# Performance work log

Hardware: AMD Instinct MI355X
Metric: run time of the kernel (lower is better)

Reference implementation:

```python
import jax, jax.numpy as jnp
import numpy as np

N = 100000
E = 3200000
D_IN = 512
D_HID = 128
D_OUT = 4


def setup_inputs() -> dict:
    key = jax.random.key(0)
    k1, k2, k3, k4, k5, k6 = jax.random.split(key, 6)
    x = jax.random.normal(k1, (N, D_IN), dtype=jnp.float32)
    edge_index = jax.random.randint(k2, (2, E), 0, N, dtype=jnp.int64)
    # GCNConv params (Glorot-ish scale)
    W1 = jax.random.normal(k3, (D_IN, D_HID), dtype=jnp.float32) / np.sqrt(D_IN)
    b1 = jax.random.normal(k4, (D_HID,), dtype=jnp.float32) * 0.01
    W2 = jax.random.normal(k5, (D_HID, D_OUT), dtype=jnp.float32) / np.sqrt(D_HID)
    b2 = jax.random.normal(k6, (D_OUT,), dtype=jnp.float32) * 0.01
    return {"x": x, "edge_index": edge_index, "W1": W1, "b1": b1, "W2": W2, "b2": b2}


def _gcn_conv(x, W, b, src, dst, deg_inv_sqrt):
    # h = X W, then symmetric-normalized aggregation with self-loops (PyG GCNConv default)
    h = x @ W                                   # [N, F_out]
    norm = deg_inv_sqrt[src] * deg_inv_sqrt[dst]  # [E]
    agg = jax.ops.segment_sum(h[src] * norm[:, None], dst, num_segments=x.shape[0])
    # self-loop contribution: norm_ii = deg_inv_sqrt[i]^2
    agg = agg + h * (deg_inv_sqrt ** 2)[:, None]
    return agg + b


def reference(x, edge_index, W1, b1, W2, b2):
    src, dst = edge_index[0], edge_index[1]
    # degree with added self-loops (edge weights = 1)
    deg = jax.ops.segment_sum(jnp.ones((E,), dtype=x.dtype), dst, num_segments=N) + 1.0
    deg_inv_sqrt = jax.lax.rsqrt(deg)
    h = jax.nn.relu(_gcn_conv(x, W1, b1, src, dst, deg_inv_sqrt))
    out = _gcn_conv(h, W2, b2, src, dst, deg_inv_sqrt)
    return out
```

## Files before the change

kernel.cpp:

```cpp
#include <hip/hip_runtime.h>
#include <hip/hip_fp16.h>

#define DIN 512
#define DHID 128
#define DOUT 4
#define BSH 8
#define PA_CHUNK 8192
#define AST 72

typedef _Float16 f16x8 __attribute__((ext_vector_type(8)));
typedef _Float16 f16x4 __attribute__((ext_vector_type(4)));
typedef float    f32x4 __attribute__((ext_vector_type(4)));

__global__ void detect_i64_k(const int* __restrict__ raw, int* __restrict__ flag) {
  if (blockIdx.x == 0 && threadIdx.x == 0) {
    int z = 1;
    for (int k = 0; k < 8; ++k)
      if (raw[2 * k + 1] != 0) z = 0;
    flag[0] = z;
  }
}

__global__ __launch_bounds__(256) void bcount_k(const int* __restrict__ raw,
                                                const int* __restrict__ flag,
                                                int* __restrict__ gbcnt, int E) {
  __shared__ int h[512];
  const int tid = threadIdx.x;
  const int f = flag[0];
  for (int i = tid; i < 512; i += 256) h[i] = 0;
  __syncthreads();
  const size_t e0 = (size_t)blockIdx.x * PA_CHUNK;
  #pragma unroll
  for (int k = 0; k < 32; ++k) {
    size_t e = e0 + (size_t)k * 256 + tid;
    if (e < (size_t)E) {
      int d = f ? raw[2 * ((size_t)E + e)] : raw[(size_t)E + e];
      atomicAdd(&h[d >> BSH], 1);
    }
  }
  __syncthreads();
  for (int i = tid; i < 512; i += 256)
    if (h[i]) atomicAdd(&gbcnt[i], h[i]);
}

__global__ __launch_bounds__(512) void bscan_k(const int* __restrict__ gbcnt,
                                               int* __restrict__ boffs,
                                               int* __restrict__ bcur,
                                               int* __restrict__ offs,
                                               int nbkt, int N, int E) {
  __shared__ int sm[512];
  int t = threadIdx.x;
  int v = (t < nbkt) ? gbcnt[t] : 0;
  int x = v;
  sm[t] = x;
  __syncthreads();
  #pragma unroll
  for (int o = 1; o < 512; o <<= 1) {
    int y = (t >= o) ? sm[t - o] : 0;
    __syncthreads();
    x += y;
    sm[t] = x;
    __syncthreads();
  }
  if (t < nbkt) {
    boffs[t] = x - v;
    bcur[t] = x - v;
  }
  if (t == 0) {
    boffs[nbkt] = E;
    offs[N] = E;
  }
}

__global__ __launch_bounds__(256) void binA_k(const int* __restrict__ raw,
                                              const int* __restrict__ flag,
                                              int* __restrict__ bcur,
                                              unsigned* __restrict__ pairs, int E) {
  __shared__ int hist[512];
  __shared__ int base[512];
  const int tid = threadIdx.x;
  const int f = flag[0];
  const size_t e0 = (size_t)blockIdx.x * PA_CHUNK;
  for (int i = tid; i < 512; i += 256) hist[i] = 0;
  __syncthreads();
  int es[32], ed[32];
  #pragma unroll
  for (int k = 0; k < 32; ++k) {
    size_t e = e0 + (size_t)k * 256 + tid;
    if (e < (size_t)E) {
      es[k] = f ? raw[2 * e] : raw[e];
      ed[k] = f ? raw[2 * ((size_t)E + e)] : raw[(size_t)E + e];
      atomicAdd(&hist[ed[k] >> BSH], 1);
    } else {
      ed[k] = -1;
    }
  }
  __syncthreads();
  for (int i = tid; i < 512; i += 256) {
    int c = hist[i];
    base[i] = c ? atomicAdd(&bcur[i], c) : 0;
    hist[i] = 0;
  }
  __syncthreads();
  #pragma unroll
  for (int k = 0; k < 32; ++k) {
    if (ed[k] >= 0) {
      int b = ed[k] >> BSH;
      int pos = base[b] + atomicAdd(&hist[b], 1);
      pairs[pos] = ((unsigned)es[k] << 8) | ((unsigned)ed[k] & 255u);
    }
  }
}

__global__ __launch_bounds__(256) void binB_k(const unsigned* __restrict__ pairs,
                                              const int* __restrict__ boffs,
                                              int* __restrict__ csr,
                                              int* __restrict__ offs,
                                              float* __restrict__ dis, int N) {
  __shared__ int lcnt[256];
  __shared__ int sc[256];
  const int tid = threadIdx.x;
  const int n0 = blockIdx.x << BSH;
  const int lo = boffs[blockIdx.x];
  const int hi = boffs[blockIdx.x + 1];
  lcnt[tid] = 0;
  __syncthreads();
  for (int j = lo + tid; j < hi; j += 256) atomicAdd(&lcnt[(int)(pairs[j] & 255u)], 1);
  __syncthreads();
  int v = lcnt[tid];
  int x = v;
  sc[tid] = x;
  __syncthreads();
  #pragma unroll
  for (int o = 1; o < 256; o <<= 1) {
    int y = (tid >= o) ? sc[tid - o] : 0;
    __syncthreads();
    x += y;
    sc[tid] = x;
    __syncthreads();
  }
  const int base = lo + x - v;
  const int node = n0 + tid;
  if (node < N) {
    offs[node] = base;
    dis[node] = rsqrtf((float)v + 1.0f);
  }
  __syncthreads();
  lcnt[tid] = base;
  __syncthreads();
  for (int j = lo + tid; j < hi; j += 256) {
    unsigned p = pairs[j];
    int dl = (int)(p & 255u);
    int pos = atomicAdd(&lcnt[dl], 1);
    csr[pos] = (int)(p >> 8);
  }
}

__global__ __launch_bounds__(256) void wsplit_k(const float* __restrict__ W1,
                                                __half* __restrict__ Wth,
                                                __half* __restrict__ Wtl) {
  int idx = blockIdx.x * 256 + threadIdx.x;
  if (idx >= DIN * DHID) return;
  int k = idx >> 7;
  int n = idx & 127;
  float w = W1[idx];
  _Float16 hi = (_Float16)w;
  _Float16 lo = (_Float16)(w - (float)hi);
  Wth[(size_t)n * DIN + k] = *(__half*)&hi;
  Wtl[(size_t)n * DIN + k] = *(__half*)&lo;
}

__global__ __launch_bounds__(256, 2) void gemm1_k(const float* __restrict__ A,
                                                  const __half* __restrict__ Bth,
                                                  const __half* __restrict__ Btl,
                                                  const float* __restrict__ dis,
                                                  __half* __restrict__ hs, int N) {
  __shared__ _Float16 smem[4 * 128 * AST];
  __shared__ float sdis[128];
  _Float16* sAh = smem;
  _Float16* sAl = smem + 128 * AST;
  _Float16* sBh = smem + 2 * 128 * AST;
  _Float16* sBl = smem + 3 * 128 * AST;
  const int tid = threadIdx.x;
  const int wave = tid >> 6, lane = tid & 63;
  const int lr = lane & 15, quad = lane >> 4;
  const int m0 = blockIdx.x * 128;
  const int mbase = (wave >> 1) * 64;
  const int nbase = (wave & 1) * 64;
  if (tid < 128) sdis[tid] = (m0 + tid < N) ? dis[m0 + tid] : 0.f;

  f32x4 acc[4][4];
  #pragma unroll
  for (int mt = 0; mt < 4; ++mt)
    #pragma unroll
    for (int nt = 0; nt < 4; ++nt) acc[mt][nt] = (f32x4){0.f, 0.f, 0.f, 0.f};

  for (int k0 = 0; k0 < DIN; k0 += 64) {
    #pragma unroll
    for (int l = 0; l < 8; ++l) {
      int idx = l * 256 + tid;
      int row = idx >> 4;
      int kk = (idx & 15) << 2;
      int gr = m0 + row;
      float4 v = make_float4(0.f, 0.f, 0.f, 0.f);
      if (gr < N) v = *(const float4*)(A + (size_t)gr * DIN + k0 + kk);
      _Float16 h0 = (_Float16)v.x, h1 = (_Float16)v.y,
               h2 = (_Float16)v.z, h3 = (_Float16)v.w;
      f16x4 hi4 = {h0, h1, h2, h3};
      f16x4 lo4 = {(_Float16)(v.x - (float)h0), (_Float16)(v.y - (float)h1),
                   (_Float16)(v.z - (float)h2), (_Float16)(v.w - (float)h3)};
      *(f16x4*)&sAh[row * AST + kk] = hi4;
      *(f16x4*)&sAl[row * AST + kk] = lo4;
    }
    #pragma unroll
    for (int l = 0; l < 4; ++l) {
      int idx = l * 256 + tid;
      int row = idx >> 3;
      int kk = (idx & 7) << 3;
      *(f16x8*)&sBh[row * AST + kk] =
          *(const f16x8*)(Bth + (size_t)row * DIN + k0 + kk);
      *(f16x8*)&sBl[row * AST + kk] =
          *(const f16x8*)(Btl + (size_t)row * DIN + k0 + kk);
    }
    __syncthreads();
    #pragma unroll
    for (int ks = 0; ks < 2; ++ks) {
      const int ko = ks * 32 + quad * 8;
      f16x8 ah[4], al[4];
      #pragma unroll
      for (int mt = 0; mt < 4; ++mt) {
        int r = mbase + mt * 16 + lr;
        ah[mt] = *(const f16x8*)&sAh[r * AST + ko];
        al[mt] = *(const f16x8*)&sAl[r * AST + ko];
      }
      #pragma unroll
      for (int nt = 0; nt < 4; ++nt) {
        int c = nbase + nt * 16 + lr;
        f16x8 bh = *(const f16x8*)&sBh[c * AST + ko];
        f16x8 bl = *(const f16x8*)&sBl[c * AST + ko];
        #pragma unroll
        for (int mt = 0; mt < 4; ++mt) {
          acc[mt][nt] = __builtin_amdgcn_mfma_f32_16x16x32_f16(al[mt], bh, acc[mt][nt], 0, 0, 0);
          acc[mt][nt] = __builtin_amdgcn_mfma_f32_16x16x32_f16(ah[mt], bl, acc[mt][nt], 0, 0, 0);
          acc[mt][nt] = __builtin_amdgcn_mfma_f32_16x16x32_f16(ah[mt], bh, acc[mt][nt], 0, 0, 0);
        }
      }
    }
    __syncthreads();
  }
  #pragma unroll
  for (int mt = 0; mt < 4; ++mt) {
    #pragma unroll
    for (int nt = 0; nt < 4; ++nt) {
      int col = nbase + nt * 16 + lr;
      #pragma unroll
      for (int r = 0; r < 4; ++r) {
        int row = mbase + mt * 16 + quad * 4 + r;
        smem[row * 136 + col] = (_Float16)(acc[mt][nt][r] * sdis[row]);
      }
    }
  }
  __syncthreads();
  #pragma unroll
  for (int l = 0; l < 8; ++l) {
    int idx = l * 256 + tid;
    int row = idx >> 4;
    int c = (idx & 15) << 3;
    int gr = m0 + row;
    if (gr < N)
      *(uint4*)(hs + (size_t)gr * DHID + c) = *(uint4*)&smem[row * 136 + c];
  }
}

__global__ __launch_bounds__(256) void agg1_k(const __half* __restrict__ hs,
                                              const float* __restrict__ dis,
                                              const int* __restrict__ offs,
                                              const int* __restrict__ csr,
                                              const float* __restrict__ W2,
                                              const float* __restrict__ b1,
                                              float* __restrict__ gs, int N) {
  const int wid = threadIdx.x >> 6;
  const int lane = threadIdx.x & 63;
  const int i = blockIdx.x * 4 + wid;
  if (i >= N) return;
  const int f = lane * 2;
  const __half* hp = hs + f;
  float ax = 0.f, ay = 0.f;
  const int beg = offs[i], end = offs[i + 1];
  for (int base = beg; base < end; base += 64) {
    int sj = 0;
    if (base + lane < end) sj = csr[base + lane];
    const int n = min(64, end - base);
    int t = 0;
    for (; t + 8 <= n; t += 8) {
      int s0 = __shfl(sj, t + 0, 64), s1 = __shfl(sj, t + 1, 64);
      int s2 = __shfl(sj, t + 2, 64), s3 = __shfl(sj, t + 3, 64);
      int s4 = __shfl(sj, t + 4, 64), s5 = __shfl(sj, t + 5, 64);
      int s6 = __shfl(sj, t + 6, 64), s7 = __shfl(sj, t + 7, 64);
      __half2 h0 = *(const __half2*)(hp + (size_t)s0 * DHID);
      __half2 h1 = *(const __half2*)(hp + (size_t)s1 * DHID);
      __half2 h2 = *(const __half2*)(hp + (size_t)s2 * DHID);
      __half2 h3 = *(const __half2*)(hp + (size_t)s3 * DHID);
      __half2 h4 = *(const __half2*)(hp + (size_t)s4 * DHID);
      __half2 h5 = *(const __half2*)(hp + (size_t)s5 * DHID);
      __half2 h6 = *(const __half2*)(hp + (size_t)s6 * DHID);
      __half2 h7 = *(const __half2*)(hp + (size_t)s7 * DHID);
      float2 f0 = __half22float2(h0), f1 = __half22float2(h1);
      float2 f2 = __half22float2(h2), f3 = __half22float2(h3);
      float2 f4 = __half22float2(h4), f5 = __half22float2(h5);
      float2 f6 = __half22float2(h6), f7 = __half22float2(h7);
      ax += ((f0.x + f1.x) + (f2.x + f3.x)) + ((f4.x + f5.x) + (f6.x + f7.x));
      ay += ((f0.y + f1.y) + (f2.y + f3.y)) + ((f4.y + f5.y) + (f6.y + f7.y));
    }
    for (; t < n; ++t) {
      int s = __shfl(sj, t, 64);
      float2 hf = __half22float2(*(const __half2*)(hp + (size_t)s * DHID));
      ax += hf.x;
      ay += hf.y;
    }
  }
  {
    float2 hf = __half22float2(*(const __half2*)(hp + (size_t)i * DHID));
    ax += hf.x;
    ay += hf.y;
  }
  const float di = dis[i];
  float v0 = fmaxf(fmaf(ax, di, b1[f]), 0.f);
  float v1 = fmaxf(fmaf(ay, di, b1[f + 1]), 0.f);
  float p0 = fmaf(v0, W2[f * 4 + 0], v1 * W2[f * 4 + 4]);
  float p1 = fmaf(v0, W2[f * 4 + 1], v1 * W2[f * 4 + 5]);
  float p2 = fmaf(v0, W2[f * 4 + 2], v1 * W2[f * 4 + 6]);
  float p3 = fmaf(v0, W2[f * 4 + 3], v1 * W2[f * 4 + 7]);
  #pragma unroll
  for (int o = 32; o > 0; o >>= 1) {
    p0 += __shfl_xor(p0, o, 64);
    p1 += __shfl_xor(p1, o, 64);
    p2 += __shfl_xor(p2, o, 64);
    p3 += __shfl_xor(p3, o, 64);
  }
  if (lane == 0)
    *(float4*)(gs + (size_t)i * DOUT) = make_float4(p0 * di, p1 * di, p2 * di, p3 * di);
}

__global__ __launch_bounds__(256) void agg2_k(const float* __restrict__ gs,
                                              const float* __restrict__ dis,
                                              const int* __restrict__ offs,
                                              const int* __restrict__ csr,
                                              const float* __restrict__ b2,
                                              float* __restrict__ out, int N) {
  int i = blockIdx.x * 256 + threadIdx.x;
  if (i >= N) return;
  float a0 = 0.f, a1 = 0.f, a2 = 0.f, a3 = 0.f;
  const int beg = offs[i], end = offs[i + 1];
  int j = beg;
  for (; j + 4 <= end; j += 4) {
    int s0 = csr[j], s1 = csr[j + 1], s2 = csr[j + 2], s3 = csr[j + 3];
    float4 g0 = *(const float4*)(gs + (size_t)s0 * DOUT);
    float4 g1 = *(const float4*)(gs + (size_t)s1 * DOUT);
    float4 g2 = *(const float4*)(gs + (size_t)s2 * DOUT);
    float4 g3 = *(const float4*)(gs + (size_t)s3 * DOUT);
    a0 += (g0.x + g1.x) + (g2.x + g3.x);
    a1 += (g0.y + g1.y) + (g2.y + g3.y);
    a2 += (g0.z + g1.z) + (g2.z + g3.z);
    a3 += (g0.w + g1.w) + (g2.w + g3.w);
  }
  for (; j < end; ++j) {
    int s = csr[j];
    float4 gv = *(const float4*)(gs + (size_t)s * DOUT);
    a0 += gv.x; a1 += gv.y; a2 += gv.z; a3 += gv.w;
  }
  const float di = dis[i];
  float4 gi = *(const float4*)(gs + (size_t)i * DOUT);
  float4 o4;
  o4.x = fmaf(a0 + gi.x, di, b2[0]);
  o4.y = fmaf(a1 + gi.y, di, b2[1]);
  o4.z = fmaf(a2 + gi.z, di, b2[2]);
  o4.w = fmaf(a3 + gi.w, di, b2[3]);
  *(float4*)(out + (size_t)i * DOUT) = o4;
}

extern "C" void kernel_launch(void* const* d_in, const int* in_sizes, int n_in,
                              void* d_out, int out_size, void* d_ws, size_t ws_size,
                              hipStream_t stream) {
  const float* x  = (const float*)d_in[0];
  const int*   raw = (const int*)d_in[1];
  const float* W1 = (const float*)d_in[2];
  const float* b1 = (const float*)d_in[3];
  const float* W2 = (const float*)d_in[4];
  const float* b2 = (const float*)d_in[5];
  float* out = (float*)d_out;

  const int N = in_sizes[0] / DIN;
  const int E = in_sizes[1] / 2;

  char* ws = (char*)d_ws;
  size_t off = 0;
  auto carve = [&](size_t bytes) -> char* {
    char* p = ws + off;
    off = (off + bytes + 255) & ~(size_t)255;
    return p;
  };
  float*    dis  = (float*)carve((size_t)N * 4);
  int*      offs = (int*)carve((size_t)(N + 1) * 4);
  int*      csr  = (int*)carve((size_t)E * 4);
  unsigned* pairs= (unsigned*)carve((size_t)E * 4);
  int*      boffs= (int*)carve(513 * 4);
  int*      bcur = (int*)carve(512 * 4);
  int*      gbcnt= (int*)carve(512 * 4);
  int*      flag = (int*)carve(256);
  __half*   Wth  = (__half*)carve((size_t)DIN * DHID * 2);
  __half*   Wtl  = (__half*)carve((size_t)DIN * DHID * 2);
  __half*   hs   = (__half*)carve((size_t)N * DHID * 2);
  float*    gs   = (float*)carve((size_t)N * DOUT * 4);
  (void)ws_size; (void)n_in; (void)out_size;

  const int gN = (N + 255) / 256;
  const int nbkt = (N + (1 << BSH) - 1) >> BSH;
  const int gA = (E + PA_CHUNK - 1) / PA_CHUNK;

  detect_i64_k<<<1, 64, 0, stream>>>(raw, flag);
  hipMemsetAsync(gbcnt, 0, 512 * 4, stream);
  bcount_k<<<gA, 256, 0, stream>>>(raw, flag, gbcnt, E);
  bscan_k<<<1, 512, 0, stream>>>(gbcnt, boffs, bcur, offs, nbkt, N, E);
  binA_k<<<gA, 256, 0, stream>>>(raw, flag, bcur, pairs, E);
  binB_k<<<nbkt, 256, 0, stream>>>(pairs, boffs, csr, offs, dis, N);
  wsplit_k<<<(DIN * DHID + 255) / 256, 256, 0, stream>>>(W1, Wth, Wtl);
  gemm1_k<<<(N + 127) / 128, 256, 0, stream>>>(x, Wth, Wtl, dis, hs, N);
  agg1_k<<<(N + 3) / 4, 256, 0, stream>>>(hs, dis, offs, csr, W2, b1, gs, N);
  agg2_k<<<gN, 256, 0, stream>>>(gs, dis, offs, csr, b2, out, N);
}
```

Measured before the change: 571.5 us.

## Register-prefetch next K-slice in gemm1 with smaller tiles for higher occupancy

The GEMM1 K-step drops from 64 to 32, which shrinks the LDS tiles (BST 40) and raises launch bounds to 3 blocks per CU. Global loads for the next K-slice go into registers before the MFMA work on the current slice, so memory latency overlaps compute. The dis shared buffer is removed and dis is read straight from global in the epilogue. In exchange there are twice as many barriers per K loop and more register pressure, which could cause spills under the 3-block bound.

```diff
diff --git a/kernel.cpp b/kernel.cpp
--- a/kernel.cpp
+++ b/kernel.cpp
@@ -6,7 +6,7 @@
 #define DOUT 4
 #define BSH 8
 #define PA_CHUNK 8192
-#define AST 72
+#define BST 40
 
 typedef _Float16 f16x8 __attribute__((ext_vector_type(8)));
 typedef _Float16 f16x4 __attribute__((ext_vector_type(4)));
@@ -170,24 +170,50 @@
   Wtl[(size_t)n * DIN + k] = *(__half*)&lo;
 }
 
-__global__ __launch_bounds__(256, 2) void gemm1_k(const float* __restrict__ A,
+#define STAGE_A(v, l)                                                          \
+  {                                                                            \
+    _Float16 h0 = (_Float16)(v).x, h1 = (_Float16)(v).y,                       \
+             h2 = (_Float16)(v).z, h3 = (_Float16)(v).w;                       \
+    f16x4 hi4 = {h0, h1, h2, h3};                                              \
+    f16x4 lo4 = {(_Float16)((v).x - (float)h0), (_Float16)((v).y - (float)h1), \
+                 (_Float16)((v).z - (float)h2), (_Float16)((v).w - (float)h3)};\
+    *(f16x4*)&sAh[((l) * 32 + ar) * BST + akk] = hi4;                          \
+    *(f16x4*)&sAl[((l) * 32 + ar) * BST + akk] = lo4;                          \
+  }
+
+__global__ __launch_bounds__(256, 3) void gemm1_k(const float* __restrict__ A,
                                                   const __half* __restrict__ Bth,
                                                   const __half* __restrict__ Btl,
                                                   const float* __restrict__ dis,
                                                   __half* __restrict__ hs, int N) {
-  __shared__ _Float16 smem[4 * 128 * AST];
-  __shared__ float sdis[128];
+  __shared__ _Float16 smem[4 * 128 * BST];
   _Float16* sAh = smem;
-  _Float16* sAl = smem + 128 * AST;
-  _Float16* sBh = smem + 2 * 128 * AST;
-  _Float16* sBl = smem + 3 * 128 * AST;
+  _Float16* sAl = smem + 128 * BST;
+  _Float16* sBh = smem + 2 * 128 * BST;
+  _Float16* sBl = smem + 3 * 128 * BST;
   const int tid = threadIdx.x;
   const int wave = tid >> 6, lane = tid & 63;
   const int lr = lane & 15, quad = lane >> 4;
   const int m0 = blockIdx.x * 128;
   const int mbase = (wave >> 1) * 64;
   const int nbase = (wave & 1) * 64;
-  if (tid < 128) sdis[tid] = (m0 + tid < N) ? dis[m0 + tid] : 0.f;
+
+  const int ar  = tid >> 3;
+  const int akk = (tid & 7) << 2;
+  const int br0 = tid >> 2;
+  const int br1 = (256 + tid) >> 2;
+  const int bcc = (tid & 3) << 3;
+
+  const int g0 = m0 + ar,      g1 = m0 + 32 + ar;
+  const int g2 = m0 + 64 + ar, g3 = m0 + 96 + ar;
+  const float* a0p = A + (size_t)g0 * DIN + akk;
+  const float* a1p = A + (size_t)g1 * DIN + akk;
+  const float* a2p = A + (size_t)g2 * DIN + akk;
+  const float* a3p = A + (size_t)g3 * DIN + akk;
+  const __half* bh0p = Bth + (size_t)br0 * DIN + bcc;
+  const __half* bh1p = Bth + (size_t)br1 * DIN + bcc;
+  const __half* bl0p = Btl + (size_t)br0 * DIN + bcc;
+  const __half* bl1p = Btl + (size_t)br1 * DIN + bcc;
 
   f32x4 acc[4][4];
   #pragma unroll
@@ -195,68 +221,73 @@
     #pragma unroll
     for (int nt = 0; nt < 4; ++nt) acc[mt][nt] = (f32x4){0.f, 0.f, 0.f, 0.f};
 
-  for (int k0 = 0; k0 < DIN; k0 += 64) {
+  const float4 z4 = make_float4(0.f, 0.f, 0.f, 0.f);
+  float4 pa0 = (g0 < N) ? *(const float4*)a0p : z4;
+  float4 pa1 = (g1 < N) ? *(const float4*)a1p : z4;
+  float4 pa2 = (g2 < N) ? *(const float4*)a2p : z4;
+  float4 pa3 = (g3 < N) ? *(const float4*)a3p : z4;
+  uint4 pbh0 = *(const uint4*)bh0p;
+  uint4 pbh1 = *(const uint4*)bh1p;
+  uint4 pbl0 = *(const uint4*)bl0p;
+  uint4 pbl1 = *(const uint4*)bl1p;
+
+  for (int k0 = 0; k0 < DIN; k0 += 32) {
+    STAGE_A(pa0, 0);
+    STAGE_A(pa1, 1);
+    STAGE_A(pa2, 2);
+    STAGE_A(pa3, 3);
+    *(uint4*)&sBh[br0 * BST + bcc] = pbh0;
+    *(uint4*)&sBh[br1 * BST + bcc] = pbh1;
+    *(uint4*)&sBl[br0 * BST + bcc] = pbl0;
+    *(uint4*)&sBl[br1 * BST + bcc] = pbl1;
+    __syncthreads();
+    if (k0 + 32 < DIN) {
+      const int k1 = k0 + 32;
+      pa0 = (g0 < N) ? *(const float4*)(a0p + k1) : z4;
+      pa1 = (g1 < N) ? *(const float4*)(a1p + k1) : z4;
+      pa2 = (g2 < N) ? *(const float4*)(a2p + k1) : z4;
+      pa3 = (g3 < N) ? *(const float4*)(a3p + k1) : z4;
+      pbh0 = *(const uint4*)(bh0p + k1);
+      pbh1 = *(const uint4*)(bh1p + k1);
+      pbl0 = *(const uint4*)(bl0p + k1);
+      pbl1 = *(const uint4*)(bl1p + k1);
+    }
+    const int ko = quad * 8;
+    f16x8 ah[4], al[4];
     #pragma unroll
-    for (int l = 0; l < 8; ++l) {
-      int idx = l * 256 + tid;
-      int row = idx >> 4;
-      int kk = (idx & 15) << 2;
+    for (int mt = 0; mt < 4; ++mt) {
+      int r = mbase + mt * 16 + lr;
+      ah[mt] = *(const f16x8*)&sAh[r * BST + ko];
+      al[mt] = *(const f16x8*)&sAl[r * BST + ko];
+    }
+    #pragma unroll
+    for (int nt = 0; nt < 4; ++nt) {
+      int c = nbase + nt * 16 + lr;
+      f16x8 bh = *(const f16x8*)&sBh[c * BST + ko];
+      f16x8 bl = *(const f16x8*)&sBl[c * BST + ko];
+      #pragma unroll
+      for (int mt = 0; mt < 4; ++mt)
+        acc[mt][nt] = __builtin_amdgcn_mfma_f32_16x16x32_f16(al[mt], bh, acc[mt][nt], 0, 0, 0);
+      #pragma unroll
+      for (int mt = 0; mt < 4; ++mt)
+        acc[mt][nt] = __builtin_amdgcn_mfma_f32_16x16x32_f16(ah[mt], bl, acc[mt][nt], 0, 0, 0);
+      #pragma unroll
+      for (int mt = 0; mt < 4; ++mt)
+        acc[mt][nt] = __builtin_amdgcn_mfma_f32_16x16x32_f16(ah[mt], bh, acc[mt][nt], 0, 0, 0);
+    }
+    __syncthreads();
+  }
+  #pragma unroll
+  for (int mt = 0; mt < 4; ++mt) {
+    #pragma unroll
+    for (int r = 0; r < 4; ++r) {
+      int row = mbase + mt * 16 + quad * 4 + r;
       int gr = m0 + row;
-      float4 v = make_float4(0.f, 0.f, 0.f, 0.f);
-      if (gr < N) v = *(const float4*)(A + (size_t)gr * DIN + k0 + kk);
-      _Float16 h0 = (_Float16)v.x, h1 = (_Float16)v.y,
-               h2 = (_Float16)v.z, h3 = (_Float16)v.w;
-      f16x4 hi4 = {h0, h1, h2, h3};
-      f16x4 lo4 = {(_Float16)(v.x - (float)h0), (_Float16)(v.y - (float)h1),
-                   (_Float16)(v.z - (float)h2), (_Float16)(v.w - (float)h3)};
-      *(f16x4*)&sAh[row * AST + kk] = hi4;
-      *(f16x4*)&sAl[row * AST + kk] = lo4;
-    }
-    #pragma unroll
-    for (int l = 0; l < 4; ++l) {
-      int idx = l * 256 + tid;
-      int row = idx >> 3;
-      int kk = (idx & 7) << 3;
-      *(f16x8*)&sBh[row * AST + kk] =
-          *(const f16x8*)(Bth + (size_t)row * DIN + k0 + kk);
-      *(f16x8*)&sBl[row * AST + kk] =
-          *(const f16x8*)(Btl + (size_t)row * DIN + k0 + kk);
-    }
-    __syncthreads();
-    #pragma unroll
-    for (int ks = 0; ks < 2; ++ks) {
-      const int ko = ks * 32 + quad * 8;
-      f16x8 ah[4], al[4];
-      #pragma unroll
-      for (int mt = 0; mt < 4; ++mt) {
-        int r = mbase + mt * 16 + lr;
-        ah[mt] = *(const f16x8*)&sAh[r * AST + ko];
-        al[mt] = *(const f16x8*)&sAl[r * AST + ko];
-      }
+      float dv = dis[gr < N ? gr : (N - 1)];
       #pragma unroll
       for (int nt = 0; nt < 4; ++nt) {
-        int c = nbase + nt * 16 + lr;
-        f16x8 bh = *(const f16x8*)&sBh[c * AST + ko];
-        f16x8 bl = *(const f16x8*)&sBl[c * AST + ko];
-        #pragma unroll
-        for (int mt = 0; mt < 4; ++mt) {
-          acc[mt][nt] = __builtin_amdgcn_mfma_f32_16x16x32_f16(al[mt], bh, acc[mt][nt], 0, 0, 0);
-          acc[mt][nt] = __builtin_amdgcn_mfma_f32_16x16x32_f16(ah[mt], bl, acc[mt][nt], 0, 0, 0);
-          acc[mt][nt] = __builtin_amdgcn_mfma_f32_16x16x32_f16(ah[mt], bh, acc[mt][nt], 0, 0, 0);
-        }
-      }
-    }
-    __syncthreads();
-  }
-  #pragma unroll
-  for (int mt = 0; mt < 4; ++mt) {
-    #pragma unroll
-    for (int nt = 0; nt < 4; ++nt) {
-      int col = nbase + nt * 16 + lr;
-      #pragma unroll
-      for (int r = 0; r < 4; ++r) {
-        int row = mbase + mt * 16 + quad * 4 + r;
-        smem[row * 136 + col] = (_Float16)(acc[mt][nt][r] * sdis[row]);
+        int col = nbase + nt * 16 + lr;
+        smem[row * 136 + col] = (_Float16)(acc[mt][nt][r] * dv);
       }
     }
   }
```

Measured after the change: 555.2 us. 2.8% less time.

## Restructure GEMM1 to load A and B fragments directly from global memory

Applied to the files above, without the earlier changes.

GEMM1 no longer stages A and B tiles through shared memory. Each wave now owns 32 rows across all 128 columns, loads its A fragments straight into registers with one-step prefetch, and reads B fragments directly from global memory, which is small and cache-resident. This removes the shared-memory staging and per-tile barriers and cuts LDS use, so occupancy is raised to 3 blocks per CU. The cost is redundant B reads from L1/L2 by every wave and less reuse of B across rows.

```diff
diff --git a/kernel.cpp b/kernel.cpp
--- a/kernel.cpp
+++ b/kernel.cpp
@@ -6,7 +6,6 @@
 #define DOUT 4
 #define BSH 8
 #define PA_CHUNK 8192
-#define AST 72
 
 typedef _Float16 f16x8 __attribute__((ext_vector_type(8)));
 typedef _Float16 f16x4 __attribute__((ext_vector_type(4)));
@@ -170,93 +169,93 @@
   Wtl[(size_t)n * DIN + k] = *(__half*)&lo;
 }
 
-__global__ __launch_bounds__(256, 2) void gemm1_k(const float* __restrict__ A,
+#define CVT8(vA, vB, hi8, lo8)                                                 \
+  {                                                                            \
+    _Float16 c0 = (_Float16)(vA).x, c1 = (_Float16)(vA).y,                     \
+             c2 = (_Float16)(vA).z, c3 = (_Float16)(vA).w,                     \
+             c4 = (_Float16)(vB).x, c5 = (_Float16)(vB).y,                     \
+             c6 = (_Float16)(vB).z, c7 = (_Float16)(vB).w;                     \
+    hi8 = (f16x8){c0, c1, c2, c3, c4, c5, c6, c7};                             \
+    lo8 = (f16x8){(_Float16)((vA).x - (float)c0), (_Float16)((vA).y - (float)c1), \
+                  (_Float16)((vA).z - (float)c2), (_Float16)((vA).w - (float)c3), \
+                  (_Float16)((vB).x - (float)c4), (_Float16)((vB).y - (float)c5), \
+                  (_Float16)((vB).z - (float)c6), (_Float16)((vB).w - (float)c7)};\
+  }
+
+__global__ __launch_bounds__(256, 3) void gemm1_k(const float* __restrict__ A,
                                                   const __half* __restrict__ Bth,
                                                   const __half* __restrict__ Btl,
                                                   const float* __restrict__ dis,
                                                   __half* __restrict__ hs, int N) {
-  __shared__ _Float16 smem[4 * 128 * AST];
-  __shared__ float sdis[128];
-  _Float16* sAh = smem;
-  _Float16* sAl = smem + 128 * AST;
-  _Float16* sBh = smem + 2 * 128 * AST;
-  _Float16* sBl = smem + 3 * 128 * AST;
+  __shared__ _Float16 smem[128 * 136];
   const int tid = threadIdx.x;
   const int wave = tid >> 6, lane = tid & 63;
   const int lr = lane & 15, quad = lane >> 4;
   const int m0 = blockIdx.x * 128;
-  const int mbase = (wave >> 1) * 64;
-  const int nbase = (wave & 1) * 64;
-  if (tid < 128) sdis[tid] = (m0 + tid < N) ? dis[m0 + tid] : 0.f;
-
-  f32x4 acc[4][4];
-  #pragma unroll
-  for (int mt = 0; mt < 4; ++mt)
+  const int r0 = m0 + wave * 32 + lr;
+  const int r1 = r0 + 16;
+
+  const float* a0p = A + (size_t)r0 * DIN + quad * 8;
+  const float* a1p = A + (size_t)r1 * DIN + quad * 8;
+  const __half* bhp = Bth + (size_t)lr * DIN + quad * 8;
+  const __half* blp = Btl + (size_t)lr * DIN + quad * 8;
+
+  f32x4 acc[2][8];
+  #pragma unroll
+  for (int mt = 0; mt < 2; ++mt)
     #pragma unroll
-    for (int nt = 0; nt < 4; ++nt) acc[mt][nt] = (f32x4){0.f, 0.f, 0.f, 0.f};
-
-  for (int k0 = 0; k0 < DIN; k0 += 64) {
+    for (int j = 0; j < 8; ++j) acc[mt][j] = (f32x4){0.f, 0.f, 0.f, 0.f};
+
+  const float4 z4 = make_float4(0.f, 0.f, 0.f, 0.f);
+  const bool v0 = (r0 < N), v1 = (r1 < N);
+  float4 pa00 = v0 ? *(const float4*)(a0p)     : z4;
+  float4 pa01 = v0 ? *(const float4*)(a0p + 4) : z4;
+  float4 pa10 = v1 ? *(const float4*)(a1p)     : z4;
+  float4 pa11 = v1 ? *(const float4*)(a1p + 4) : z4;
+
+  for (int k0 = 0; k0 < DIN; k0 += 32) {
+    f16x8 ah0, al0, ah1, al1;
+    CVT8(pa00, pa01, ah0, al0);
+    CVT8(pa10, pa11, ah1, al1);
+    if (k0 + 32 < DIN) {
+      const int k1 = k0 + 32;
+      pa00 = v0 ? *(const float4*)(a0p + k1)     : z4;
+      pa01 = v0 ? *(const float4*)(a0p + k1 + 4) : z4;
+      pa10 = v1 ? *(const float4*)(a1p + k1)     : z4;
+      pa11 = v1 ? *(const float4*)(a1p + k1 + 4) : z4;
+    }
     #pragma unroll
-    for (int l = 0; l < 8; ++l) {
-      int idx = l * 256 + tid;
-      int row = idx >> 4;
-      int kk = (idx & 15) << 2;
-      int gr = m0 + row;
-      float4 v = make_float4(0.f, 0.f, 0.f, 0.f);
-      if (gr < N) v = *(const float4*)(A + (size_t)gr * DIN + k0 + kk);
-      _Float16 h0 = (_Float16)v.x, h1 = (_Float16)v.y,
-               h2 = (_Float16)v.z, h3 = (_Float16)v.w;
-      f16x4 hi4 = {h0, h1, h2, h3};
-      f16x4 lo4 = {(_Float16)(v.x - (float)h0), (_Float16)(v.y - (float)h1),
-                   (_Float16)(v.z - (float)h2), (_Float16)(v.w - (float)h3)};
-      *(f16x4*)&sAh[row * AST + kk] = hi4;
-      *(f16x4*)&sAl[row * AST + kk] = lo4;
-    }
-    #pragma unroll
-    for (int l = 0; l < 4; ++l) {
-      int idx = l * 256 + tid;
-      int row = idx >> 3;
-      int kk = (idx & 7) << 3;
-      *(f16x8*)&sBh[row * AST + kk] =
-          *(const f16x8*)(Bth + (size_t)row * DIN + k0 + kk);
-      *(f16x8*)&sBl[row * AST + kk] =
-          *(const f16x8*)(Btl + (size_t)row * DIN + k0 + kk);
-    }
-    __syncthreads();
-    #pragma unroll
-    for (int ks = 0; ks < 2; ++ks) {
-      const int ko = ks * 32 + quad * 8;
-      f16x8 ah[4], al[4];
+    for (int h = 0; h < 2; ++h) {
+      f16x8 bh[4], bl[4];
       #pragma unroll
-      for (int mt = 0; mt < 4; ++mt) {
-        int r = mbase + mt * 16 + lr;
-        ah[mt] = *(const f16x8*)&sAh[r * AST + ko];
-        al[mt] = *(const f16x8*)&sAl[r * AST + ko];
+      for (int nt = 0; nt < 4; ++nt) {
+        const size_t co = (size_t)(h * 4 + nt) * 16 * DIN + k0;
+        bh[nt] = *(const f16x8*)(bhp + co);
+        bl[nt] = *(const f16x8*)(blp + co);
       }
       #pragma unroll
       for (int nt = 0; nt < 4; ++nt) {
-        int c = nbase + nt * 16 + lr;
-        f16x8 bh = *(const f16x8*)&sBh[c * AST + ko];
-        f16x8 bl = *(const f16x8*)&sBl[c * AST + ko];
-        #pragma unroll
-        for (int mt = 0; mt < 4; ++mt) {
-          acc[mt][nt] = __builtin_amdgcn_mfma_f32_16x16x32_f16(al[mt], bh, acc[mt][nt], 0, 0, 0);
-          acc[mt][nt] = __builtin_amdgcn_mfma_f32_16x16x32_f16(ah[mt], bl, acc[mt][nt], 0, 0, 0);
-          acc[mt][nt] = __builtin_amdgcn_mfma_f32_16x16x32_f16(ah[mt], bh, acc[mt][nt], 0, 0, 0);
-        }
+        const int j = h * 4 + nt;
+        acc[0][j] = __builtin_amdgcn_mfma_f32_16x16x32_f16(al0, bh[nt], acc[0][j], 0, 0, 0);
+        acc[0][j] = __builtin_amdgcn_mfma_f32_16x16x32_f16(ah0, bl[nt], acc[0][j], 0, 0, 0);
+        acc[0][j] = __builtin_amdgcn_mfma_f32_16x16x32_f16(ah0, bh[nt], acc[0][j], 0, 0, 0);
+        acc[1][j] = __builtin_amdgcn_mfma_f32_16x16x32_f16(al1, bh[nt], acc[1][j], 0, 0, 0);
+        acc[1][j] = __builtin_amdgcn_mfma_f32_16x16x32_f16(ah1, bl[nt], acc[1][j], 0, 0, 0);
+        acc[1][j] = __builtin_amdgcn_mfma_f32_16x16x32_f16(ah1, bh[nt], acc[1][j], 0, 0, 0);
       }
     }
-    __syncthreads();
-  }
-  #pragma unroll
-  for (int mt = 0; mt < 4; ++mt) {
+  }
+  #pragma unroll
+  for (int mt = 0; mt < 2; ++mt) {
     #pragma unroll
-    for (int nt = 0; nt < 4; ++nt) {
-      int col = nbase + nt * 16 + lr;
+    for (int r = 0; r < 4; ++r) {
+      int row = wave * 32 + mt * 16 + quad * 4 + r;
+      int gr = m0 + row;
+      float dv = dis[gr < N ? gr : (N - 1)];
       #pragma unroll
-      for (int r = 0; r < 4; ++r) {
-        int row = mbase + mt * 16 + quad * 4 + r;
-        smem[row * 136 + col] = (_Float16)(acc[mt][nt][r] * sdis[row]);
+      for (int j = 0; j < 8; ++j) {
+        int col = j * 16 + lr;
+        smem[row * 136 + col] = (_Float16)(acc[mt][j][r] * dv);
       }
     }
   }
```

Result: slower. 686.4 us (+20.1%).

## Load GEMM tiles directly into LDS with swizzled layout and split A in registers

Applied to the files above, without the earlier changes.

The first-layer GEMM now uses global_load_lds to copy fp32 A tiles and a pre-interleaved hi/lo fp16 weight layout straight into shared memory, using an XOR swizzle instead of padding. The fp16 hi/lo split of A moves from the staging store to register time after the LDS read. The K tile shrinks to 32 so LDS use drops and occupancy rises to 4 blocks per CU, and the dis scale is read from global memory in the epilogue. This is meant to cut VGPR round-trips and LDS footprint in the memory-bound x load, but it adds more barriers per K step and repeats the conversion work for every wave that reads a row.

```diff
diff --git a/kernel.cpp b/kernel.cpp
--- a/kernel.cpp
+++ b/kernel.cpp
@@ -6,11 +6,15 @@
 #define DOUT 4
 #define BSH 8
 #define PA_CHUNK 8192
-#define AST 72
 
 typedef _Float16 f16x8 __attribute__((ext_vector_type(8)));
 typedef _Float16 f16x4 __attribute__((ext_vector_type(4)));
 typedef float    f32x4 __attribute__((ext_vector_type(4)));
+
+#define GLOAD_LDS(gp, lp)                                                     \
+  __builtin_amdgcn_global_load_lds(                                           \
+      (const __attribute__((address_space(1))) void*)(gp),                    \
+      (__attribute__((address_space(3))) void*)(lp), 16, 0, 0)
 
 __global__ void detect_i64_k(const int* __restrict__ raw, int* __restrict__ flag) {
   if (blockIdx.x == 0 && threadIdx.x == 0) {
@@ -157,37 +161,34 @@
 }
 
 __global__ __launch_bounds__(256) void wsplit_k(const float* __restrict__ W1,
-                                                __half* __restrict__ Wth,
-                                                __half* __restrict__ Wtl) {
+                                                __half* __restrict__ Bt2) {
   int idx = blockIdx.x * 256 + threadIdx.x;
   if (idx >= DIN * DHID) return;
   int k = idx >> 7;
   int n = idx & 127;
+  int kt = k >> 5, kk = k & 31;
   float w = W1[idx];
   _Float16 hi = (_Float16)w;
   _Float16 lo = (_Float16)(w - (float)hi);
-  Wth[(size_t)n * DIN + k] = *(__half*)&hi;
-  Wtl[(size_t)n * DIN + k] = *(__half*)&lo;
-}
-
-__global__ __launch_bounds__(256, 2) void gemm1_k(const float* __restrict__ A,
-                                                  const __half* __restrict__ Bth,
-                                                  const __half* __restrict__ Btl,
+  size_t base = (size_t)(kt * 128 + n) * 64;
+  Bt2[base + kk]      = *(__half*)&hi;
+  Bt2[base + 32 + kk] = *(__half*)&lo;
+}
+
+__global__ __launch_bounds__(256, 4) void gemm1_k(const float* __restrict__ A,
+                                                  const __half* __restrict__ Bt2,
                                                   const float* __restrict__ dis,
                                                   __half* __restrict__ hs, int N) {
-  __shared__ _Float16 smem[4 * 128 * AST];
-  __shared__ float sdis[128];
-  _Float16* sAh = smem;
-  _Float16* sAl = smem + 128 * AST;
-  _Float16* sBh = smem + 2 * 128 * AST;
-  _Float16* sBl = smem + 3 * 128 * AST;
+  __shared__ _Float16 smem[128 * 136];
+  char* sAc = (char*)smem;
+  char* sBc = (char*)smem + 16384;
   const int tid = threadIdx.x;
   const int wave = tid >> 6, lane = tid & 63;
   const int lr = lane & 15, quad = lane >> 4;
   const int m0 = blockIdx.x * 128;
   const int mbase = (wave >> 1) * 64;
   const int nbase = (wave & 1) * 64;
-  if (tid < 128) sdis[tid] = (m0 + tid < N) ? dis[m0 + tid] : 0.f;
+  const int wbase = (tid & ~63) * 16;
 
   f32x4 acc[4][4];
   #pragma unroll
@@ -195,68 +196,74 @@
     #pragma unroll
     for (int nt = 0; nt < 4; ++nt) acc[mt][nt] = (f32x4){0.f, 0.f, 0.f, 0.f};
 
-  for (int k0 = 0; k0 < DIN; k0 += 64) {
-    #pragma unroll
-    for (int l = 0; l < 8; ++l) {
-      int idx = l * 256 + tid;
-      int row = idx >> 4;
-      int kk = (idx & 15) << 2;
+  int arow[4], achk[4];
+  #pragma unroll
+  for (int l = 0; l < 4; ++l) {
+    int d16 = l * 256 + tid;
+    int row = d16 >> 3;
+    arow[l] = row;
+    achk[l] = (d16 & 7) ^ (row & 7);
+  }
+
+  for (int kt = 0; kt < 16; ++kt) {
+    const int k0 = kt * 32;
+    #pragma unroll
+    for (int l = 0; l < 4; ++l) {
+      int gr = m0 + arow[l];
+      if (gr >= N) gr = N - 1;
+      GLOAD_LDS(A + (size_t)gr * DIN + k0 + achk[l] * 4,
+                sAc + (size_t)l * 4096 + wbase);
+    }
+    #pragma unroll
+    for (int l = 0; l < 4; ++l) {
+      GLOAD_LDS(Bt2 + (size_t)(kt * 128 + arow[l]) * 64 + achk[l] * 8,
+                sBc + (size_t)l * 4096 + wbase);
+    }
+    __syncthreads();
+    f16x8 ah[4], al[4];
+    #pragma unroll
+    for (int mt = 0; mt < 4; ++mt) {
+      int r = mbase + mt * 16 + lr;
+      f32x4 v0 = *(const f32x4*)(sAc + r * 128 + (((2 * quad + 0) ^ (r & 7)) << 4));
+      f32x4 v1 = *(const f32x4*)(sAc + r * 128 + (((2 * quad + 1) ^ (r & 7)) << 4));
+      _Float16 c0 = (_Float16)v0[0], c1 = (_Float16)v0[1],
+               c2 = (_Float16)v0[2], c3 = (_Float16)v0[3],
+               c4 = (_Float16)v1[0], c5 = (_Float16)v1[1],
+               c6 = (_Float16)v1[2], c7 = (_Float16)v1[3];
+      ah[mt] = (f16x8){c0, c1, c2, c3, c4, c5, c6, c7};
+      al[mt] = (f16x8){(_Float16)(v0[0] - (float)c0), (_Float16)(v0[1] - (float)c1),
+                       (_Float16)(v0[2] - (float)c2), (_Float16)(v0[3] - (float)c3),
+                       (_Float16)(v1[0] - (float)c4), (_Float16)(v1[1] - (float)c5),
+                       (_Float16)(v1[2] - (float)c6), (_Float16)(v1[3] - (float)c7)};
+    }
+    #pragma unroll
+    for (int nt = 0; nt < 4; ++nt) {
+      int c = nbase + nt * 16 + lr;
+      f16x8 bh = *(const f16x8*)(sBc + c * 128 + (((0 + quad) ^ (c & 7)) << 4));
+      f16x8 bl = *(const f16x8*)(sBc + c * 128 + (((4 + quad) ^ (c & 7)) << 4));
+      #pragma unroll
+      for (int mt = 0; mt < 4; ++mt)
+        acc[mt][nt] = __builtin_amdgcn_mfma_f32_16x16x32_f16(al[mt], bh, acc[mt][nt], 0, 0, 0);
+      #pragma unroll
+      for (int mt = 0; mt < 4; ++mt)
+        acc[mt][nt] = __builtin_amdgcn_mfma_f32_16x16x32_f16(ah[mt], bl, acc[mt][nt], 0, 0, 0);
+      #pragma unroll
+      for (int mt = 0; mt < 4; ++mt)
+        acc[mt][nt] = __builtin_amdgcn_mfma_f32_16x16x32_f16(ah[mt], bh, acc[mt][nt], 0, 0, 0);
+    }
+    __syncthreads();
+  }
+  #pragma unroll
+  for (int mt = 0; mt < 4; ++mt) {
+    #pragma unroll
+    for (int r = 0; r < 4; ++r) {
+      int row = mbase + mt * 16 + quad * 4 + r;
       int gr = m0 + row;
-      float4 v = make_float4(0.f, 0.f, 0.f, 0.f);
-      if (gr < N) v = *(const float4*)(A + (size_t)gr * DIN + k0 + kk);
-      _Float16 h0 = (_Float16)v.x, h1 = (_Float16)v.y,
-               h2 = (_Float16)v.z, h3 = (_Float16)v.w;
-      f16x4 hi4 = {h0, h1, h2, h3};
-      f16x4 lo4 = {(_Float16)(v.x - (float)h0), (_Float16)(v.y - (float)h1),
-                   (_Float16)(v.z - (float)h2), (_Float16)(v.w - (float)h3)};
-      *(f16x4*)&sAh[row * AST + kk] = hi4;
-      *(f16x4*)&sAl[row * AST + kk] = lo4;
-    }
-    #pragma unroll
-    for (int l = 0; l < 4; ++l) {
-      int idx = l * 256 + tid;
-      int row = idx >> 3;
-      int kk = (idx & 7) << 3;
-      *(f16x8*)&sBh[row * AST + kk] =
-          *(const f16x8*)(Bth + (size_t)row * DIN + k0 + kk);
-      *(f16x8*)&sBl[row * AST + kk] =
-          *(const f16x8*)(Btl + (size_t)row * DIN + k0 + kk);
-    }
-    __syncthreads();
-    #pragma unroll
-    for (int ks = 0; ks < 2; ++ks) {
-      const int ko = ks * 32 + quad * 8;
-      f16x8 ah[4], al[4];
-      #pragma unroll
-      for (int mt = 0; mt < 4; ++mt) {
-        int r = mbase + mt * 16 + lr;
-        ah[mt] = *(const f16x8*)&sAh[r * AST + ko];
-        al[mt] = *(const f16x8*)&sAl[r * AST + ko];
-      }
+      float dv = dis[gr < N ? gr : (N - 1)];
       #pragma unroll
       for (int nt = 0; nt < 4; ++nt) {
-        int c = nbase + nt * 16 + lr;
-        f16x8 bh = *(const f16x8*)&sBh[c * AST + ko];
-        f16x8 bl = *(const f16x8*)&sBl[c * AST + ko];
-        #pragma unroll
-        for (int mt = 0; mt < 4; ++mt) {
-          acc[mt][nt] = __builtin_amdgcn_mfma_f32_16x16x32_f16(al[mt], bh, acc[mt][nt], 0, 0, 0);
-          acc[mt][nt] = __builtin_amdgcn_mfma_f32_16x16x32_f16(ah[mt], bl, acc[mt][nt], 0, 0, 0);
-          acc[mt][nt] = __builtin_amdgcn_mfma_f32_16x16x32_f16(ah[mt], bh, acc[mt][nt], 0, 0, 0);
-        }
-      }
-    }
-    __syncthreads();
-  }
-  #pragma unroll
-  for (int mt = 0; mt < 4; ++mt) {
-    #pragma unroll
-    for (int nt = 0; nt < 4; ++nt) {
-      int col = nbase + nt * 16 + lr;
-      #pragma unroll
-      for (int r = 0; r < 4; ++r) {
-        int row = mbase + mt * 16 + quad * 4 + r;
-        smem[row * 136 + col] = (_Float16)(acc[mt][nt][r] * sdis[row]);
+        int col = nbase + nt * 16 + lr;
+        smem[row * 136 + col] = (_Float16)(acc[mt][nt][r] * dv);
       }
     }
   }
@@ -408,8 +415,7 @@
   int*      bcur = (int*)carve(512 * 4);
   int*      gbcnt= (int*)carve(512 * 4);
   int*      flag = (int*)carve(256);
-  __half*   Wth  = (__half*)carve((size_t)DIN * DHID * 2);
-  __half*   Wtl  = (__half*)carve((size_t)DIN * DHID * 2);
+  __half*   Bt2  = (__half*)carve((size_t)DIN * DHID * 2 * 2);
   __half*   hs   = (__half*)carve((size_t)N * DHID * 2);
   float*    gs   = (float*)carve((size_t)N * DOUT * 4);
   (void)ws_size; (void)n_in; (void)out_size;
@@ -424,8 +430,8 @@
   bscan_k<<<1, 512, 0, stream>>>(gbcnt, boffs, bcur, offs, nbkt, N, E);
   binA_k<<<gA, 256, 0, stream>>>(raw, flag, bcur, pairs, E);
   binB_k<<<nbkt, 256, 0, stream>>>(pairs, boffs, csr, offs, dis, N);
-  wsplit_k<<<(DIN * DHID + 255) / 256, 256, 0, stream>>>(W1, Wth, Wtl);
-  gemm1_k<<<(N + 127) / 128, 256, 0, stream>>>(x, Wth, Wtl, dis, hs, N);
+  wsplit_k<<<(DIN * DHID + 255) / 256, 256, 0, stream>>>(W1, Bt2);
+  gemm1_k<<<(N + 127) / 128, 256, 0, stream>>>(x, Bt2, dis, hs, N);
   agg1_k<<<(N + 3) / 4, 256, 0, stream>>>(hs, dis, offs, csr, W2, b1, gs, N);
   agg2_k<<<gN, 256, 0, stream>>>(gs, dis, offs, csr, b2, out, N);
 }
```

Result: faster. 535.3 us (-6.3%).
